# Optimization experiments

Hardware: AMD Instinct MI355X
Metric: run time of the kernel (lower is better)

## Reference

```python
import jax, jax.numpy as jnp
import numpy as np

EPS = 1e-5


def conv2d(x, w, b, pad):
    # x: [B,C,H,W], w: [O,I,kh,kw]
    out = jax.lax.conv_general_dilated(
        x, w, window_strides=(1, 1), padding=[(pad, pad), (pad, pad)],
        dimension_numbers=('NCHW', 'OIHW', 'NCHW'))
    return out + b[None, :, None, None]


def bilinear_gather(xf, py, px, H, W):
    # xf: [B,C,H*W]; py,px: [B,H,W] float sampling positions
    # zero padding outside the image (torchvision deform_conv2d semantics)
    y0 = jnp.floor(py)
    x0 = jnp.floor(px)
    wy = py - y0
    wx = px - x0
    y0i = y0.astype(jnp.int32)
    x0i = x0.astype(jnp.int32)
    B, C = xf.shape[0], xf.shape[1]
    acc = jnp.zeros((B, C, H, W), xf.dtype)
    for dy, wyv in ((0, 1.0 - wy), (1, wy)):
        for dx, wxv in ((0, 1.0 - wx), (1, wx)):
            yi = y0i + dy
            xi = x0i + dx
            valid = ((yi >= 0) & (yi < H) & (xi >= 0) & (xi < W)).astype(xf.dtype)
            idx = jnp.clip(yi, 0, H - 1) * W + jnp.clip(xi, 0, W - 1)  # [B,H,W]
            g = jnp.take_along_axis(xf, idx.reshape(B, 1, H * W), axis=2)
            g = g.reshape(B, C, H, W)
            acc = acc + g * (wyv * wxv * valid)[:, None]
    return acc


def deform_conv2d(x, offset, w, b, k):
    # x: [B,C,H,W]; offset: [B,2*k*k,H,W] ((dy,dx) pairs per kernel tap)
    B, C, H, W = x.shape
    pad = k // 2
    gy = jnp.arange(H, dtype=x.dtype)[None, :, None]
    gx = jnp.arange(W, dtype=x.dtype)[None, None, :]
    xf = x.reshape(B, C, H * W)
    out = jnp.zeros((B, w.shape[0], H, W), x.dtype)
    for i in range(k):
        for j in range(k):
            kk = i * k + j
            py = gy + (i - pad) + offset[:, 2 * kk]
            px = gx + (j - pad) + offset[:, 2 * kk + 1]
            samp = bilinear_gather(xf, py, px, H, W)  # [B,C,H,W]
            out = out + jnp.einsum('bchw,oc->bohw', samp, w[:, :, i, j])
    return out + b[None, :, None, None]


def setup_inputs() -> dict:
    key = jax.random.key(0)
    ks = jax.random.split(key, 16)
    B, C, H, W = 4, 64, 192, 192
    k = 3
    hid = max(1, C // 16)
    d = {}
    d['x'] = jax.random.normal(ks[0], (B, C, H, W), jnp.float32)
    # offset-prediction conv (3x3, pad 1) -> 2*k*k channels
    d['off_w'] = jax.random.normal(ks[1], (2 * k * k, C, 3, 3), jnp.float32) * 0.02
    d['off_b'] = jax.random.normal(ks[2], (2 * k * k,), jnp.float32) * 0.02
    # deformable conv weights (C->C, kxk)
    d['dw'] = jax.random.normal(ks[3], (C, C, k, k), jnp.float32) * 0.05
    d['db'] = jax.random.normal(ks[4], (C,), jnp.float32) * 0.05
    # BatchNorm (eval: running stats)
    d['bn_gamma'] = jnp.ones((C,), jnp.float32) + 0.1 * jax.random.normal(ks[5], (C,), jnp.float32)
    d['bn_beta'] = 0.1 * jax.random.normal(ks[6], (C,), jnp.float32)
    d['bn_mean'] = 0.1 * jax.random.normal(ks[7], (C,), jnp.float32)
    d['bn_var'] = jnp.ones((C,), jnp.float32)
    # channel attention: 1x1 squeeze / excite
    d['ca_w1'] = jax.random.normal(ks[8], (hid, C, 1, 1), jnp.float32) * 0.1
    d['ca_b1'] = jnp.zeros((hid,), jnp.float32)
    d['ca_w2'] = jax.random.normal(ks[9], (C, hid, 1, 1), jnp.float32) * 0.1
    d['ca_b2'] = jnp.zeros((C,), jnp.float32)
    # spatial attention: 7x7 conv -> 1 channel
    d['sa_w'] = jax.random.normal(ks[10], (1, C, 7, 7), jnp.float32) * 0.02
    d['sa_b'] = jnp.zeros((1,), jnp.float32)
    return d


def reference(x, off_w, off_b, dw, db, bn_gamma, bn_beta, bn_mean, bn_var,
              ca_w1, ca_b1, ca_w2, ca_b2, sa_w, sa_b):
    k = 3
    # extract: DeformableConv2d + BatchNorm2d
    offset = conv2d(x, off_w, off_b, pad=1)
    h = deform_conv2d(x, offset, dw, db, k)
    inv = jax.lax.rsqrt(bn_var + EPS)
    h = (h - bn_mean[None, :, None, None]) * (bn_gamma * inv)[None, :, None, None] \
        + bn_beta[None, :, None, None]
    # channel attention
    pooled = jnp.mean(h, axis=(2, 3), keepdims=True)  # [B,C,1,1]
    cw = conv2d(pooled, ca_w1, ca_b1, pad=0)
    cw = jax.nn.relu(cw)
    cw = conv2d(cw, ca_w2, ca_b2, pad=0)
    cw = jax.nn.sigmoid(cw)
    h = h * cw
    # spatial attention (7x7 conv, pad 3)
    sw = jax.nn.sigmoid(conv2d(h, sa_w, sa_b, pad=3))  # [B,1,H,W]
    h = h * sw
    return h
```

## Files before the change

kernel.cpp:

```cpp
#include <hip/hip_runtime.h>
#include <hip/hip_fp16.h>

#define H_  192
#define W_  192
#define HW  36864
#define B_  4

typedef __attribute__((ext_vector_type(8))) short short8;
typedef __attribute__((ext_vector_type(4))) float f32x4;
typedef __attribute__((ext_vector_type(4))) unsigned int u32x4;
typedef unsigned short ushort_t;
typedef unsigned int uint_t;

__device__ __forceinline__ ushort_t f2h(float v) {
    __half h = __float2half(v);
    ushort_t s;
    __builtin_memcpy(&s, &h, 2);
    return s;
}
__device__ __forceinline__ float h2f(ushort_t s) {
    __half h;
    __builtin_memcpy(&h, &s, 2);
    return __half2float(h);
}
__device__ __forceinline__ __half2 u2h2(uint_t u) {
    __half2 h;
    __builtin_memcpy(&h, &u, 4);
    return h;
}
__device__ __forceinline__ uint_t h22u(__half2 h) {
    uint_t u;
    __builtin_memcpy(&u, &h, 4);
    return u;
}
__device__ __forceinline__ short8 zero8() {
    u32x4 z = {0u, 0u, 0u, 0u};
    return __builtin_bit_cast(short8, z);
}

__device__ __forceinline__ void glds16(const ushort_t* src, void* lds_base) {
    __builtin_amdgcn_global_load_lds(
        (const __attribute__((address_space(1))) void*)src,
        (__attribute__((address_space(3))) void*)lds_base, 16, 0, 0);
}

__global__ __launch_bounds__(256) void prep_transpose_kernel(
    const float* __restrict__ x, ushort_t* __restrict__ x_t,
    const float* __restrict__ dw, const float* __restrict__ db,
    const float* __restrict__ g, const float* __restrict__ be,
    const float* __restrict__ mu, const float* __restrict__ var,
    const float* __restrict__ ow,
    ushort_t* __restrict__ w_bf, ushort_t* __restrict__ w_off,
    float* __restrict__ scale, float* __restrict__ shift) {
    __shared__ uint_t tlds[256 * 33];
    int tid = threadIdx.x;

    int idx = blockIdx.x * 256 + tid;
    if (idx < 36864) {
        int tap = idx >> 12, o = (idx >> 6) & 63, c = idx & 63;
        w_bf[idx] = f2h(dw[(o * 64 + c) * 9 + tap]);
    }
    int idx2 = idx - 36864;
    if (idx2 >= 0 && idx2 < 18432) {
        int tap = idx2 >> 11, o = (idx2 >> 6) & 31, c = idx2 & 63;
        w_off[idx2] = (o < 18) ? f2h(ow[(o * 64 + c) * 9 + tap]) : (ushort_t)0;
    }
    if (idx < 64) {
        float s = g[idx] * rsqrtf(var[idx] + 1e-5f);
        scale[idx] = s;
        shift[idx] = (db[idx] - mu[idx]) * s + be[idx];
    }

    int b = blockIdx.x / 144;
    int p0 = (blockIdx.x % 144) * 256;
    ushort_t* ts = (ushort_t*)tlds;
    for (int c = 0; c < 64; ++c) {
        float v = x[((size_t)(b * 64 + c)) * HW + p0 + tid];
        ts[tid * 66 + c] = f2h(v);
    }
    __syncthreads();
#pragma unroll
    for (int j = 0; j < 8; ++j) {
        int chunk = j * 256 + tid;
        int pl = chunk >> 3, s = chunk & 7;
        int bd = pl * 33 + s * 4;
        u32x4 v = {tlds[bd], tlds[bd + 1], tlds[bd + 2], tlds[bd + 3]};
        ((u32x4*)x_t)[(size_t)(b * HW + p0) * 8 + chunk] = v;
    }
}

__device__ __forceinline__ u32x4 prd(const ushort_t* patch, int q, int slot) {
    return *(const u32x4*)((const char*)patch + q * 128 + ((slot ^ (q & 7)) << 4));
}

__device__ __forceinline__ bool corner_setup2(float ody, float odx,
                                              int ybase, int xbase, int ytop, int xleft,
                                              int* q, int* g, float* w) {
    float py = (float)ybase + ody;
    float px = (float)xbase + odx;
    float fy = floorf(py), fx = floorf(px);
    int y0 = (int)fy, x0 = (int)fx;
    float wy = py - fy, wx = px - fx;
    int y0c = min(max(y0, 0), H_ - 1), y1c = min(max(y0 + 1, 0), H_ - 1);
    int x0c = min(max(x0, 0), W_ - 1), x1c = min(max(x0 + 1, 0), W_ - 1);
    float vy0 = (y0 >= 0 && y0 < H_) ? 1.f : 0.f;
    float vy1 = (y0 + 1 >= 0 && y0 + 1 < H_) ? 1.f : 0.f;
    float vx0 = (x0 >= 0 && x0 < W_) ? 1.f : 0.f;
    float vx1 = (x0 + 1 >= 0 && x0 + 1 < W_) ? 1.f : 0.f;
    w[0] = (1.f - wy) * (1.f - wx) * vy0 * vx0;
    w[1] = (1.f - wy) * wx * vy0 * vx1;
    w[2] = wy * (1.f - wx) * vy1 * vx0;
    w[3] = wy * wx * vy1 * vx1;
    g[0] = (y0c * W_ + x0c) * 64; g[1] = (y0c * W_ + x1c) * 64;
    g[2] = (y1c * W_ + x0c) * 64; g[3] = (y1c * W_ + x1c) * 64;
    int iy0 = y0c - ytop, iy1 = y1c - ytop;
    int ix0 = x0c - xleft, ix1 = x1c - xleft;
    q[0] = iy0 * 56 + ix0; q[1] = iy0 * 56 + ix1;
    q[2] = iy1 * 56 + ix0; q[3] = iy1 * 56 + ix1;
    return ((unsigned)iy0 <= 11u) & ((unsigned)iy1 <= 11u) &
           ((unsigned)ix0 <= 55u) & ((unsigned)ix1 <= 55u);
}

__device__ __forceinline__ short8 interp_f16(const u32x4* buf, const __half2* w2) {
    short8 r;
#pragma unroll
    for (int q = 0; q < 4; ++q) {
        __half2 acc = __hmul2(u2h2(buf[0][q]), w2[0]);
        acc = __hfma2(u2h2(buf[1][q]), w2[1], acc);
        acc = __hfma2(u2h2(buf[2][q]), w2[2], acc);
        acc = __hfma2(u2h2(buf[3][q]), w2[3], acc);
        ((uint_t*)&r)[q] = h22u(acc);
    }
    return r;
}

__global__ __launch_bounds__(576, 2) void deform_fused_kernel(
    const ushort_t* __restrict__ x_t, const ushort_t* __restrict__ w_off,
    const float* __restrict__ ob, const ushort_t* __restrict__ w_bf,
    const float* __restrict__ scale_g, const float* __restrict__ shift_g,
    ushort_t* __restrict__ h16) {
    __shared__ __align__(16) ushort_t patch[672 * 64];

    int tid = threadIdx.x;
    int lane = tid & 63, w = tid >> 6;
    int tile = (blockIdx.x & 7) * 64 + (blockIdx.x >> 3);
    int b = tile / 128;
    int rem = tile % 128;
    int y0 = (rem >> 2) * 6;
    int x0 = (rem & 3) * 48;
    int ytop = y0 - 3, xleft = x0 - 4;

    int ln = lane & 15, kg = lane >> 4;
    int locA = w * 32 + ln, locB = locA + 16;
    int rowA = locA / 48, colA = locA - rowA * 48;
    int rowB = locB / 48, colB = locB - rowB * 48;
    int yA = y0 + rowA, xA = x0 + colA;
    int yB = y0 + rowB, xB = x0 + colB;
    const ushort_t* xt_b = x_t + (size_t)b * (HW * 64);

    {
        char* pbase = (char*)patch;
#pragma unroll
        for (int t = 0; t < 10; ++t) {
            if (t * 576 + w * 64 < 5376) {
                int g = t * 576 + tid;
                int q = g >> 3, sp = g & 7;
                int i = q / 56, j = q - i * 56;
                int pr = min(max(ytop + i, 0), H_ - 1);
                int pc = min(max(xleft + j, 0), W_ - 1);
                int s = sp ^ (q & 7);
                glds16(xt_b + (pr * W_ + pc) * 64 + s * 8,
                       pbase + (size_t)(t * 576 + w * 64) * 16);
            }
        }
    }
    asm volatile("s_waitcnt vmcnt(0)" ::: "memory");
    __syncthreads();

    f32x4 ao[2][2];
#pragma unroll
    for (int i = 0; i < 2; ++i)
#pragma unroll
        for (int j = 0; j < 2; ++j) ao[i][j] = (f32x4){0.f, 0.f, 0.f, 0.f};

    for (int tap = 0; tap < 9; ++tap) {
        int ti = tap / 3 - 1, tj = tap % 3 - 1;
        bool vA = ((unsigned)(yA + ti) < (unsigned)H_) && ((unsigned)(xA + tj) < (unsigned)W_);
        bool vB = ((unsigned)(yB + ti) < (unsigned)H_) && ((unsigned)(xB + tj) < (unsigned)W_);
        int qA = (rowA + 3 + ti) * 56 + (colA + 4 + tj);
        int qB = (rowB + 3 + ti) * 56 + (colB + 4 + tj);
        const ushort_t* wt = w_off + tap * 2048;
#pragma unroll
        for (int ks = 0; ks < 2; ++ks) {
            int ch = ks * 32 + kg * 8;
            int slot = kg + ks * 4;
            short8 a0 = *(const short8*)(wt + ln * 64 + ch);
            short8 a1 = *(const short8*)(wt + (16 + ln) * 64 + ch);
            short8 bA = vA ? __builtin_bit_cast(short8, prd(patch, qA, slot)) : zero8();
            short8 bB = vB ? __builtin_bit_cast(short8, prd(patch, qB, slot)) : zero8();
            ao[0][0] = __builtin_amdgcn_mfma_f32_16x16x32_f16(a0, bA, ao[0][0], 0, 0, 0);
            ao[0][1] = __builtin_amdgcn_mfma_f32_16x16x32_f16(a0, bB, ao[0][1], 0, 0, 0);
            ao[1][0] = __builtin_amdgcn_mfma_f32_16x16x32_f16(a1, bA, ao[1][0], 0, 0, 0);
            ao[1][1] = __builtin_amdgcn_mfma_f32_16x16x32_f16(a1, bB, ao[1][1], 0, 0, 0);
        }
    }

    float offA[18], offB[18];
#pragma unroll
    for (int m = 0; m < 18; ++m) {
        int src = (((m >> 2) & 3) << 4) | ln;
        float bias = ob[m];
        offA[m] = __shfl(ao[m >> 4][0][m & 3], src, 64) + bias;
        offB[m] = __shfl(ao[m >> 4][1][m & 3], src, 64) + bias;
    }

    f32x4 acc[4][2];
#pragma unroll
    for (int mt = 0; mt < 4; ++mt)
#pragma unroll
        for (int nt = 0; nt < 2; ++nt) acc[mt][nt] = (f32x4){0.f, 0.f, 0.f, 0.f};

#pragma unroll
    for (int tap = 0; tap < 9; ++tap) {
        int ti = tap / 3 - 1, tj = tap % 3 - 1;
        int qA[4], qB[4], gA[4], gB[4];
        float wA[4], wB[4];
        bool inA = corner_setup2(offA[2 * tap], offA[2 * tap + 1],
                                 yA + ti, xA + tj, ytop, xleft, qA, gA, wA);
        bool inB = corner_setup2(offB[2 * tap], offB[2 * tap + 1],
                                 yB + ti, xB + tj, ytop, xleft, qB, gB, wB);
        __half2 wA2[4], wB2[4];
#pragma unroll
        for (int c = 0; c < 4; ++c) {
            wA2[c] = __float2half2_rn(wA[c]);
            wB2[c] = __float2half2_rn(wB[c]);
        }
        const ushort_t* wt = w_bf + tap * 4096;
#pragma unroll
        for (int ks = 0; ks < 2; ++ks) {
            int ch = ks * 32 + kg * 8;
            int slot = kg + ks * 4;
            u32x4 cA[4], cB[4];
            if (__builtin_expect(inA, 1)) {
#pragma unroll
                for (int c = 0; c < 4; ++c) cA[c] = prd(patch, qA[c], slot);
            } else {
#pragma unroll
                for (int c = 0; c < 4; ++c) cA[c] = *(const u32x4*)(xt_b + gA[c] + ch);
            }
            if (__builtin_expect(inB, 1)) {
#pragma unroll
                for (int c = 0; c < 4; ++c) cB[c] = prd(patch, qB[c], slot);
            } else {
#pragma unroll
                for (int c = 0; c < 4; ++c) cB[c] = *(const u32x4*)(xt_b + gB[c] + ch);
            }
            short8 fA = interp_f16(cA, wA2);
            short8 fB = interp_f16(cB, wB2);
            short8 a0 = *(const short8*)(wt + (0 + ln) * 64 + ch);
            short8 a1 = *(const short8*)(wt + (16 + ln) * 64 + ch);
            short8 a2 = *(const short8*)(wt + (32 + ln) * 64 + ch);
            short8 a3 = *(const short8*)(wt + (48 + ln) * 64 + ch);
            acc[0][0] = __builtin_amdgcn_mfma_f32_16x16x32_f16(a0, fA, acc[0][0], 0, 0, 0);
            acc[0][1] = __builtin_amdgcn_mfma_f32_16x16x32_f16(a0, fB, acc[0][1], 0, 0, 0);
            acc[1][0] = __builtin_amdgcn_mfma_f32_16x16x32_f16(a1, fA, acc[1][0], 0, 0, 0);
            acc[1][1] = __builtin_amdgcn_mfma_f32_16x16x32_f16(a1, fB, acc[1][1], 0, 0, 0);
            acc[2][0] = __builtin_amdgcn_mfma_f32_16x16x32_f16(a2, fA, acc[2][0], 0, 0, 0);
            acc[2][1] = __builtin_amdgcn_mfma_f32_16x16x32_f16(a2, fB, acc[2][1], 0, 0, 0);
            acc[3][0] = __builtin_amdgcn_mfma_f32_16x16x32_f16(a3, fA, acc[3][0], 0, 0, 0);
            acc[3][1] = __builtin_amdgcn_mfma_f32_16x16x32_f16(a3, fB, acc[3][1], 0, 0, 0);
        }
    }

    int pixA = yA * W_ + xA;
    int pixB = yB * W_ + xB;
#pragma unroll
    for (int mt = 0; mt < 4; ++mt) {
#pragma unroll
        for (int r = 0; r < 4; ++r) {
            int m = mt * 16 + kg * 4 + r;
            float sc = scale_g[m], sh = shift_g[m];
            size_t obase = (size_t)(b * 64 + m) * HW;
            h16[obase + pixA] = f2h(acc[mt][0][r] * sc + sh);
            h16[obase + pixB] = f2h(acc[mt][1][r] * sc + sh);
        }
    }
}

__global__ __launch_bounds__(256) void pool_kernel(const ushort_t* __restrict__ h,
                                                   float* __restrict__ pooled) {
    __shared__ float red[4];
    int tid = threadIdx.x;
    const ushort_t* src = h + (size_t)blockIdx.x * HW;
    float s = 0.f;
#pragma unroll 2
    for (int i = tid * 8; i < HW; i += 2048) {
        short8 v = *(const short8*)(src + i);
#pragma unroll
        for (int q = 0; q < 8; ++q) s += h2f((ushort_t)v[q]);
    }
#pragma unroll
    for (int d = 1; d < 64; d <<= 1) s += __shfl_xor(s, d, 64);
    if ((tid & 63) == 0) red[tid >> 6] = s;
    __syncthreads();
    if (tid == 0)
        pooled[blockIdx.x] = (red[0] + red[1] + red[2] + red[3]) * (1.0f / (float)HW);
}

__global__ void ca_kernel(const float* __restrict__ pooled_g,
                          const float* __restrict__ w1, const float* __restrict__ b1,
                          const float* __restrict__ w2, const float* __restrict__ b2,
                          const float* __restrict__ saw, float* __restrict__ cw,
                          ushort_t* __restrict__ we_bf) {
    __shared__ float pooled[256];
    __shared__ float t1[16];
    int t = threadIdx.x;
    int b = t >> 6, o = t & 63;
    pooled[t] = pooled_g[t];
    __syncthreads();
    if (t < 16) {
        int bb = t >> 2, hh = t & 3;
        float a = b1[hh];
        for (int c = 0; c < 64; ++c) a += pooled[bb * 64 + c] * w1[hh * 64 + c];
        t1[t] = fmaxf(a, 0.f);
    }
    __syncthreads();
    float a = b2[o];
#pragma unroll
    for (int h2 = 0; h2 < 4; ++h2) a += t1[b * 4 + h2] * w2[o * 4 + h2];
    float cwv = 1.f / (1.f + __expf(-a));
    cw[t] = cwv;
    for (int tap = 0; tap < 64; ++tap) {
        float v = (tap < 49) ? cwv * saw[o * 49 + tap] : 0.f;
        we_bf[(b * 64 + tap) * 64 + o] = f2h(v);
    }
}

__global__ __launch_bounds__(256) void tap_gemm_kernel(
    const ushort_t* __restrict__ h, const ushort_t* __restrict__ we_bf,
    ushort_t* __restrict__ u) {
    int tid = threadIdx.x;
    int b = blockIdx.y;
    int p0 = blockIdx.x * 128;
    int wid = tid >> 6, lane = tid & 63, ln = lane & 15, kg = lane >> 4;
    int pA = p0 + wid * 32 + ln, pB = pA + 16;
    const ushort_t* hb = h + (size_t)b * 64 * HW;
    const ushort_t* wt = we_bf + b * 4096;

    f32x4 acc[4][2];
#pragma unroll
    for (int mt = 0; mt < 4; ++mt)
#pragma unroll
        for (int nt = 0; nt < 2; ++nt) acc[mt][nt] = (f32x4){0.f, 0.f, 0.f, 0.f};

#pragma unroll
    for (int ks = 0; ks < 2; ++ks) {
        int ch = ks * 32 + kg * 8;
        short8 fA, fB;
#pragma unroll
        for (int q = 0; q < 8; ++q) {
            fA[q] = (short)hb[(size_t)(ch + q) * HW + pA];
            fB[q] = (short)hb[(size_t)(ch + q) * HW + pB];
        }
        short8 a0 = *(const short8*)(wt + (0 + ln) * 64 + ch);
        short8 a1 = *(const short8*)(wt + (16 + ln) * 64 + ch);
        short8 a2 = *(const short8*)(wt + (32 + ln) * 64 + ch);
        short8 a3 = *(const short8*)(wt + (48 + ln) * 64 + ch);
        acc[0][0] = __builtin_amdgcn_mfma_f32_16x16x32_f16(a0, fA, acc[0][0], 0, 0, 0);
        acc[0][1] = __builtin_amdgcn_mfma_f32_16x16x32_f16(a0, fB, acc[0][1], 0, 0, 0);
        acc[1][0] = __builtin_amdgcn_mfma_f32_16x16x32_f16(a1, fA, acc[1][0], 0, 0, 0);
        acc[1][1] = __builtin_amdgcn_mfma_f32_16x16x32_f16(a1, fB, acc[1][1], 0, 0, 0);
        acc[2][0] = __builtin_amdgcn_mfma_f32_16x16x32_f16(a2, fA, acc[2][0], 0, 0, 0);
        acc[2][1] = __builtin_amdgcn_mfma_f32_16x16x32_f16(a2, fB, acc[2][1], 0, 0, 0);
        acc[3][0] = __builtin_amdgcn_mfma_f32_16x16x32_f16(a3, fA, acc[3][0], 0, 0, 0);
        acc[3][1] = __builtin_amdgcn_mfma_f32_16x16x32_f16(a3, fB, acc[3][1], 0, 0, 0);
    }
#pragma unroll
    for (int mt = 0; mt < 4; ++mt)
#pragma unroll
        for (int r = 0; r < 4; ++r) {
            int m = mt * 16 + kg * 4 + r;
            if (m < 49) {
                ushort_t* up = u + (size_t)(b * 49 + m) * HW;
                up[pA] = f2h(acc[mt][0][r]);
                up[pB] = f2h(acc[mt][1][r]);
            }
        }
}

__global__ __launch_bounds__(256) void sa_final_kernel(
    float* __restrict__ out, const ushort_t* __restrict__ h,
    const ushort_t* __restrict__ u,
    const float* __restrict__ cw, const float* __restrict__ sab) {
    __shared__ float cw_l[64];
    int tid = threadIdx.x;
    int b = blockIdx.y;
    int p = blockIdx.x * 256 + tid;
    if (tid < 64) cw_l[tid] = cw[b * 64 + tid];
    __syncthreads();
    int y = p / 192, x = p - y * 192;
    float s = sab[0];
    const ushort_t* ub = u + (size_t)b * 49 * HW;
#pragma unroll
    for (int dy = 0; dy < 7; ++dy)
#pragma unroll
        for (int dx = 0; dx < 7; ++dx) {
            int yy = y + dy - 3, xx = x + dx - 3;
            bool ok = ((unsigned)yy < 192u) && ((unsigned)xx < 192u);
            int ad = ok ? (p + (dy - 3) * 192 + (dx - 3)) : 0;
            float v = h2f(ub[(size_t)(dy * 7 + dx) * HW + ad]);
            s += ok ? v : 0.f;
        }
    float swv = 1.f / (1.f + __expf(-s));
#pragma unroll 8
    for (int c = 0; c < 64; ++c) {
        size_t ix = (size_t)(b * 64 + c) * HW + p;
        out[ix] = h2f(h[ix]) * (cw_l[c] * swv);
    }
}

extern "C" void kernel_launch(void* const* d_in, const int* in_sizes, int n_in,
                              void* d_out, int out_size, void* d_ws, size_t ws_size,
                              hipStream_t stream) {
    const float* x     = (const float*)d_in[0];
    const float* off_w = (const float*)d_in[1];
    const float* off_b = (const float*)d_in[2];
    const float* dw    = (const float*)d_in[3];
    const float* db    = (const float*)d_in[4];
    const float* bn_g  = (const float*)d_in[5];
    const float* bn_b  = (const float*)d_in[6];
    const float* bn_m  = (const float*)d_in[7];
    const float* bn_v  = (const float*)d_in[8];
    const float* ca_w1 = (const float*)d_in[9];
    const float* ca_b1 = (const float*)d_in[10];
    const float* ca_w2 = (const float*)d_in[11];
    const float* ca_b2 = (const float*)d_in[12];
    const float* sa_w  = (const float*)d_in[13];
    const float* sa_b  = (const float*)d_in[14];
    float* out = (float*)d_out;
    float* ws  = (float*)d_ws;

    ushort_t* x_t    = (ushort_t*)ws;
    ushort_t* u      = (ushort_t*)ws;
    ushort_t* h16    = (ushort_t*)(ws + 4718592);
    ushort_t* w_bf   = (ushort_t*)(ws + 9437184);
    ushort_t* w_off  = (ushort_t*)(ws + 9455616);
    ushort_t* we_bf  = (ushort_t*)(ws + 9455616);
    float* scale     = ws + 9464832;
    float* shift     = ws + 9464896;
    float* cw        = ws + 9464960;
    float* pooled    = ws + 9465216;

    prep_transpose_kernel<<<576, 256, 0, stream>>>(x, x_t, dw, db, bn_g, bn_b, bn_m,
                                                   bn_v, off_w, w_bf, w_off, scale, shift);
    deform_fused_kernel<<<512, 576, 0, stream>>>(x_t, w_off, off_b, w_bf,
                                                 scale, shift, h16);
    pool_kernel<<<256, 256, 0, stream>>>(h16, pooled);
    ca_kernel<<<1, 256, 0, stream>>>(pooled, ca_w1, ca_b1, ca_w2, ca_b2, sa_w, cw, we_bf);
    tap_gemm_kernel<<<dim3(288, 4), 256, 0, stream>>>(h16, we_bf, u);
    sa_final_kernel<<<dim3(144, 4), 256, 0, stream>>>(out, h16, u, cw, sa_b);
}
```

Baseline: 121.0 us.

## Store intermediate feature map channel-last (NHWC) for vectorized access across kernels

Changes the fp16 intermediate h16 from channel-planar to pixel-major, channel-contiguous layout. The deform kernel now writes packed 8-byte stores per pixel, tap_gemm loads its B operand as a single 16-byte vector instead of eight strided scalar loads, and the final kernel reads channels as vectors. Pooling becomes a two-stage reduction: per-chunk partial sums that the CA kernel then combines. The final output writes stay channel-strided per pixel, and pooling now needs an extra reduction pass inside ca_kernel.

```diff
diff --git a/kernel.cpp b/kernel.cpp
--- a/kernel.cpp
+++ b/kernel.cpp
@@ -274,40 +274,69 @@
 
     int pixA = yA * W_ + xA;
     int pixB = yB * W_ + xB;
+    ushort_t* hA = h16 + ((size_t)b * HW + pixA) * 64 + kg * 4;
+    ushort_t* hB = h16 + ((size_t)b * HW + pixB) * 64 + kg * 4;
 #pragma unroll
     for (int mt = 0; mt < 4; ++mt) {
-#pragma unroll
-        for (int r = 0; r < 4; ++r) {
-            int m = mt * 16 + kg * 4 + r;
-            float sc = scale_g[m], sh = shift_g[m];
-            size_t obase = (size_t)(b * 64 + m) * HW;
-            h16[obase + pixA] = f2h(acc[mt][0][r] * sc + sh);
-            h16[obase + pixB] = f2h(acc[mt][1][r] * sc + sh);
-        }
-    }
-}
-
-__global__ __launch_bounds__(256) void pool_kernel(const ushort_t* __restrict__ h,
-                                                   float* __restrict__ pooled) {
-    __shared__ float red[4];
+        int m0 = mt * 16 + kg * 4;
+        float s0 = scale_g[m0], s1 = scale_g[m0 + 1], s2 = scale_g[m0 + 2], s3 = scale_g[m0 + 3];
+        float t0 = shift_g[m0], t1 = shift_g[m0 + 1], t2 = shift_g[m0 + 2], t3 = shift_g[m0 + 3];
+        {
+            uint_t lo = (uint_t)f2h(acc[mt][0][0] * s0 + t0) |
+                        ((uint_t)f2h(acc[mt][0][1] * s1 + t1) << 16);
+            uint_t hi = (uint_t)f2h(acc[mt][0][2] * s2 + t2) |
+                        ((uint_t)f2h(acc[mt][0][3] * s3 + t3) << 16);
+            uint2 pk; pk.x = lo; pk.y = hi;
+            *(uint2*)(hA + mt * 16) = pk;
+        }
+        {
+            uint_t lo = (uint_t)f2h(acc[mt][1][0] * s0 + t0) |
+                        ((uint_t)f2h(acc[mt][1][1] * s1 + t1) << 16);
+            uint_t hi = (uint_t)f2h(acc[mt][1][2] * s2 + t2) |
+                        ((uint_t)f2h(acc[mt][1][3] * s3 + t3) << 16);
+            uint2 pk; pk.x = lo; pk.y = hi;
+            *(uint2*)(hB + mt * 16) = pk;
+        }
+    }
+}
+
+__global__ __launch_bounds__(256) void pool1_kernel(const ushort_t* __restrict__ h,
+                                                    float* __restrict__ partial) {
+    __shared__ float red[4 * 64];
     int tid = threadIdx.x;
-    const ushort_t* src = h + (size_t)blockIdx.x * HW;
-    float s = 0.f;
-#pragma unroll 2
-    for (int i = tid * 8; i < HW; i += 2048) {
-        short8 v = *(const short8*)(src + i);
-#pragma unroll
-        for (int q = 0; q < 8; ++q) s += h2f((ushort_t)v[q]);
-    }
-#pragma unroll
-    for (int d = 1; d < 64; d <<= 1) s += __shfl_xor(s, d, 64);
-    if ((tid & 63) == 0) red[tid >> 6] = s;
-    __syncthreads();
-    if (tid == 0)
-        pooled[blockIdx.x] = (red[0] + red[1] + red[2] + red[3]) * (1.0f / (float)HW);
-}
-
-__global__ void ca_kernel(const float* __restrict__ pooled_g,
+    int b = blockIdx.x >> 5, k = blockIdx.x & 31;
+    int cg = tid & 7, pl = tid >> 3;
+    int p0 = k * 1152;
+    const ushort_t* hb = h + (size_t)b * HW * 64 + cg * 8;
+
+    float s[8] = {0.f, 0.f, 0.f, 0.f, 0.f, 0.f, 0.f, 0.f};
+    for (int it = 0; it < 36; ++it) {
+        int p = p0 + it * 32 + pl;
+        short8 v = *(const short8*)(hb + (size_t)p * 64);
+#pragma unroll
+        for (int q = 0; q < 8; ++q) s[q] += h2f((ushort_t)v[q]);
+    }
+#pragma unroll
+    for (int q = 0; q < 8; ++q) {
+        s[q] += __shfl_xor(s[q], 8, 64);
+        s[q] += __shfl_xor(s[q], 16, 64);
+        s[q] += __shfl_xor(s[q], 32, 64);
+    }
+    int w = tid >> 6, lane = tid & 63;
+    if (lane < 8) {
+#pragma unroll
+        for (int q = 0; q < 8; ++q) red[(w * 8 + lane) * 8 + q] = s[q];
+    }
+    __syncthreads();
+    if (tid < 64) {
+        int cgo = tid >> 3, q = tid & 7;
+        float t = red[(0 * 8 + cgo) * 8 + q] + red[(1 * 8 + cgo) * 8 + q] +
+                  red[(2 * 8 + cgo) * 8 + q] + red[(3 * 8 + cgo) * 8 + q];
+        partial[(size_t)(b * 32 + k) * 64 + tid] = t;
+    }
+}
+
+__global__ void ca_kernel(const float* __restrict__ partial,
                           const float* __restrict__ w1, const float* __restrict__ b1,
                           const float* __restrict__ w2, const float* __restrict__ b2,
                           const float* __restrict__ saw, float* __restrict__ cw,
@@ -316,7 +345,10 @@
     __shared__ float t1[16];
     int t = threadIdx.x;
     int b = t >> 6, o = t & 63;
-    pooled[t] = pooled_g[t];
+    float s = 0.f;
+#pragma unroll 4
+    for (int k = 0; k < 32; ++k) s += partial[(size_t)(b * 32 + k) * 64 + o];
+    pooled[t] = s * (1.0f / (float)HW);
     __syncthreads();
     if (t < 16) {
         int bb = t >> 2, hh = t & 3;
@@ -344,7 +376,7 @@
     int p0 = blockIdx.x * 128;
     int wid = tid >> 6, lane = tid & 63, ln = lane & 15, kg = lane >> 4;
     int pA = p0 + wid * 32 + ln, pB = pA + 16;
-    const ushort_t* hb = h + (size_t)b * 64 * HW;
+    const ushort_t* hb = h + (size_t)b * HW * 64;
     const ushort_t* wt = we_bf + b * 4096;
 
     f32x4 acc[4][2];
@@ -356,12 +388,8 @@
 #pragma unroll
     for (int ks = 0; ks < 2; ++ks) {
         int ch = ks * 32 + kg * 8;
-        short8 fA, fB;
-#pragma unroll
-        for (int q = 0; q < 8; ++q) {
-            fA[q] = (short)hb[(size_t)(ch + q) * HW + pA];
-            fB[q] = (short)hb[(size_t)(ch + q) * HW + pB];
-        }
+        short8 fA = *(const short8*)(hb + (size_t)pA * 64 + ch);
+        short8 fB = *(const short8*)(hb + (size_t)pB * 64 + ch);
         short8 a0 = *(const short8*)(wt + (0 + ln) * 64 + ch);
         short8 a1 = *(const short8*)(wt + (16 + ln) * 64 + ch);
         short8 a2 = *(const short8*)(wt + (32 + ln) * 64 + ch);
@@ -412,10 +440,16 @@
             s += ok ? v : 0.f;
         }
     float swv = 1.f / (1.f + __expf(-s));
-#pragma unroll 8
-    for (int c = 0; c < 64; ++c) {
-        size_t ix = (size_t)(b * 64 + c) * HW + p;
-        out[ix] = h2f(h[ix]) * (cw_l[c] * swv);
+    const ushort_t* hp = h + ((size_t)b * HW + p) * 64;
+#pragma unroll
+    for (int cc = 0; cc < 8; ++cc) {
+        short8 hv = *(const short8*)(hp + cc * 8);
+#pragma unroll
+        for (int q = 0; q < 8; ++q) {
+            int c = cc * 8 + q;
+            size_t ix = (size_t)(b * 64 + c) * HW + p;
+            out[ix] = h2f((ushort_t)hv[q]) * (cw_l[c] * swv);
+        }
     }
 }
 
@@ -449,14 +483,14 @@
     float* scale     = ws + 9464832;
     float* shift     = ws + 9464896;
     float* cw        = ws + 9464960;
-    float* pooled    = ws + 9465216;
+    float* partial   = ws + 9465472;
 
     prep_transpose_kernel<<<576, 256, 0, stream>>>(x, x_t, dw, db, bn_g, bn_b, bn_m,
                                                    bn_v, off_w, w_bf, w_off, scale, shift);
     deform_fused_kernel<<<512, 576, 0, stream>>>(x_t, w_off, off_b, w_bf,
                                                  scale, shift, h16);
-    pool_kernel<<<256, 256, 0, stream>>>(h16, pooled);
-    ca_kernel<<<1, 256, 0, stream>>>(pooled, ca_w1, ca_b1, ca_w2, ca_b2, sa_w, cw, we_bf);
+    pool1_kernel<<<128, 256, 0, stream>>>(h16, partial);
+    ca_kernel<<<1, 256, 0, stream>>>(partial, ca_w1, ca_b1, ca_w2, ca_b2, sa_w, cw, we_bf);
     tap_gemm_kernel<<<dim3(288, 4), 256, 0, stream>>>(h16, we_bf, u);
     sa_final_kernel<<<dim3(144, 4), 256, 0, stream>>>(out, h16, u, cw, sa_b);
 }
```

Result: slower. 133.0 us (+10.0%).
